# Kernel optimization log

Measured on AMD Instinct MI355X. Metric: run time of the kernel, lower is better.

The kernel has to match this reference:

```python
import jax, jax.numpy as jnp
import numpy as np

N = 10000
E = 320000
IN_DIM = 256
HID = 128
HEADS = 3
NEG_SLOPE = 0.2
EPS = 1e-8


def setup_inputs() -> dict:
    key = jax.random.key(0)
    ks = jax.random.split(key, 12)
    rn = lambda k, s, sc=0.1: jax.random.normal(k, s, dtype=jnp.float32) * sc
    return {
        'x1': jax.random.normal(ks[0], (N, IN_DIM), dtype=jnp.float32),
        'edge_index1': jax.random.randint(ks[1], (2, E), 0, N, dtype=jnp.int64),
        'x2': jax.random.normal(ks[2], (N, IN_DIM), dtype=jnp.float32),
        'edge_index2': jax.random.randint(ks[3], (2, E), 0, N, dtype=jnp.int64),
        'W1': rn(ks[4], (IN_DIM, HEADS * HID)),
        'att_src1': rn(ks[5], (HEADS, HID)),
        'att_dst1': rn(ks[6], (HEADS, HID)),
        'b1': rn(ks[7], (HEADS * HID,)),
        'W2': rn(ks[8], (HEADS * HID, HID)),
        'att_src2': rn(ks[9], (1, HID)),
        'att_dst2': rn(ks[10], (1, HID)),
        'b2': rn(ks[11], (HID,)),
    }


def gat_conv(x, edge_index, W, a_src, a_dst, bias, heads, out_ch, concat):
    """PyG-style GATConv with add_self_loops=True."""
    n = x.shape[0]
    loops = jnp.arange(n, dtype=edge_index.dtype)
    ei = jnp.concatenate([edge_index, jnp.stack([loops, loops])], axis=1)
    src, dst = ei[0], ei[1]
    h = (x @ W).reshape(n, heads, out_ch)                    # [N,H,C]
    s = jnp.einsum('nhc,hc->nh', h, a_src)                    # alpha_src per node
    d = jnp.einsum('nhc,hc->nh', h, a_dst)                    # alpha_dst per node
    e = jax.nn.leaky_relu(s[src] + d[dst], NEG_SLOPE)         # [Etot,H]
    m = jax.ops.segment_max(e, dst, num_segments=n)           # segment softmax (stable)
    ex = jnp.exp(e - m[dst])
    denom = jax.ops.segment_sum(ex, dst, num_segments=n)
    alpha = ex / denom[dst]                                   # [Etot,H]
    out = jax.ops.segment_sum(h[src] * alpha[:, :, None], dst, num_segments=n)
    out = out.reshape(n, heads * out_ch) if concat else out.mean(axis=1)
    return out + bias, (ei, alpha)


def _branch(x, ei, W1, as1, ad1, b1, W2, as2, ad2, b2):
    e1, (ei_sl, alpha1) = gat_conv(x, ei, W1, as1, ad1, b1, HEADS, HID, True)
    e1 = jax.nn.relu(e1)
    e2, _ = gat_conv(e1, ei, W2, as2, ad2, b2, 1, HID, False)
    # _graph_pooling
    attn_val = alpha1.mean(axis=1)                            # [Etot]
    node_attn = jax.ops.segment_sum(attn_val, ei_sl[1], num_segments=x.shape[0])
    weighted = e2 * node_attn[:, None]
    pooled = jnp.concatenate([weighted.mean(axis=0), e2.mean(axis=0)])  # [2*HID]
    return pooled, alpha1


def reference(x1, edge_index1, x2, edge_index2, W1, att_src1, att_dst1, b1,
              W2, att_src2, att_dst2, b2):
    g1, alpha1 = _branch(x1, edge_index1, W1, att_src1, att_dst1, b1,
                         W2, att_src2, att_dst2, b2)
    g2, alpha2 = _branch(x2, edge_index2, W1, att_src1, att_dst1, b1,
                         W2, att_src2, att_dst2, b2)
    n1 = jnp.maximum(jnp.linalg.norm(g1), EPS)
    n2 = jnp.maximum(jnp.linalg.norm(g2), EPS)
    sim = jnp.dot(g1, g2) / (n1 * n2)
    return sim, alpha1, alpha2
```

## Files before the change

### kernel.cpp

```cpp
#include <hip/hip_runtime.h>
#include <hip/hip_bf16.h>
#include <cstdint>
#include <cstddef>

#define INDIM 256
#define NEG 0.2f

typedef __attribute__((ext_vector_type(8))) short short8v;
typedef __attribute__((ext_vector_type(4))) float f32x4;
typedef __attribute__((ext_vector_type(2))) float f32x2;

__device__ __forceinline__ unsigned short f2bf(float x) {
  __hip_bfloat16 b = __float2bfloat16(x);
  return __builtin_bit_cast(unsigned short, b);
}

__device__ __forceinline__ unsigned char f2fp8(float v) {
  int packed = __builtin_amdgcn_cvt_pk_fp8_f32(v, v, 0, false);
  return (unsigned char)(packed & 0xff);
}

__device__ __forceinline__ float lrelu(float v) { return v > 0.f ? v : NEG * v; }

__global__ void wprep_kernel(const float* __restrict__ W1, __hip_bfloat16* __restrict__ W1t,
                             const float* __restrict__ W2, __hip_bfloat16* __restrict__ W2t) {
  int idx = blockIdx.x * blockDim.x + threadIdx.x;
  const int T1 = 256 * 384;
  if (idx < T1) {
    int k = idx / 384, c = idx - k * 384;
    W1t[(size_t)c * 256 + k] = __float2bfloat16(W1[idx]);
  } else {
    int i = idx - T1;
    if (i < 384 * 128) {
      int k = i / 128, c = i - k * 128;
      W2t[(size_t)c * 384 + k] = __float2bfloat16(W2[i]);
    }
  }
}

template<int K, bool ABF16, int SST>
__device__ __forceinline__ void gemm_body(int bx, int by,
                                          const void* __restrict__ A0,
                                          const void* __restrict__ A1, int Nsplit,
                                          const __hip_bfloat16* __restrict__ Wt,
                                          const float* __restrict__ att_s,
                                          const float* __restrict__ att_d,
                                          unsigned char* __restrict__ Yc,
                                          float* __restrict__ So,
                                          float* __restrict__ Do,
                                          int M, int NC,
                                          short (*As)[40], short (*Bs)[40],
                                          float (*sred)[64]) {
  const int tid = threadIdx.x;
  const int row0 = bx * 64;
  const int col0 = by * 128;
  const int l = tid & 63, w = tid >> 6;
  const int wr = w >> 1, wc = w & 1;
  const int lr = l & 15, lk = (l >> 4) * 8;

  f32x4 acc[2][4];
#pragma unroll
  for (int m = 0; m < 2; ++m)
#pragma unroll
    for (int n = 0; n < 4; ++n) acc[m][n] = {0.f, 0.f, 0.f, 0.f};

  for (int k0 = 0; k0 < K; k0 += 32) {
    __syncthreads();
    {
      int r = tid >> 2, kq = (tid & 3) * 8;
      int gr = row0 + r;
      short8v av = {0, 0, 0, 0, 0, 0, 0, 0};
      if (gr < M) {
        const void* Ab = (gr < Nsplit) ? A0 : A1;
        int lrow = (gr < Nsplit) ? gr : gr - Nsplit;
        if (ABF16) {
          av = *(const short8v*)((const short*)Ab + (size_t)lrow * K + k0 + kq);
        } else {
          const float* ap = (const float*)Ab + (size_t)lrow * K + k0 + kq;
          float4 u = *(const float4*)ap;
          float4 v = *(const float4*)(ap + 4);
          av = short8v{(short)f2bf(u.x), (short)f2bf(u.y), (short)f2bf(u.z), (short)f2bf(u.w),
                       (short)f2bf(v.x), (short)f2bf(v.y), (short)f2bf(v.z), (short)f2bf(v.w)};
        }
      }
      *(short8v*)&As[r][kq] = av;
    }
    {
      int c = tid >> 1, kq = (tid & 1) * 8;
      const short* wp = (const short*)Wt + (size_t)(col0 + c) * K + k0 + kq;
      *(short8v*)&Bs[c][kq]      = *(const short8v*)wp;
      *(short8v*)&Bs[c][kq + 16] = *(const short8v*)(wp + 16);
    }
    __syncthreads();
    short8v a[2], b[4];
#pragma unroll
    for (int m = 0; m < 2; ++m) a[m] = *(short8v*)&As[wr * 32 + m * 16 + lr][lk];
#pragma unroll
    for (int n = 0; n < 4; ++n) b[n] = *(short8v*)&Bs[wc * 64 + n * 16 + lr][lk];
#pragma unroll
    for (int m = 0; m < 2; ++m)
#pragma unroll
      for (int n = 0; n < 4; ++n)
        acc[m][n] = __builtin_amdgcn_mfma_f32_16x16x32_bf16(a[m], b[n], acc[m][n], 0, 0, 0);
  }
#pragma unroll
  for (int m = 0; m < 2; ++m) {
    int rbase = row0 + wr * 32 + m * 16 + (l >> 4) * 4;
#pragma unroll
    for (int n = 0; n < 4; ++n) {
      int col = col0 + wc * 64 + n * 16 + lr;
#pragma unroll
      for (int q = 0; q < 4; ++q) {
        int row = rbase + q;
        if (row < M) Yc[(size_t)row * NC + col] = f2fp8(acc[m][n][q]);
      }
    }
  }
  float asv[4], adv[4];
#pragma unroll
  for (int n = 0; n < 4; ++n) {
    int col = col0 + wc * 64 + n * 16 + lr;
    asv[n] = att_s[col];
    adv[n] = att_d[col];
  }
  float ps[2][4], pd[2][4];
#pragma unroll
  for (int m = 0; m < 2; ++m)
#pragma unroll
    for (int q = 0; q < 4; ++q) {
      float s = 0.f, d = 0.f;
#pragma unroll
      for (int n = 0; n < 4; ++n) {
        s = fmaf(acc[m][n][q], asv[n], s);
        d = fmaf(acc[m][n][q], adv[n], d);
      }
      ps[m][q] = s; pd[m][q] = d;
    }
#pragma unroll
  for (int o = 1; o < 16; o <<= 1) {
#pragma unroll
    for (int m = 0; m < 2; ++m)
#pragma unroll
      for (int q = 0; q < 4; ++q) {
        ps[m][q] += __shfl_xor(ps[m][q], o);
        pd[m][q] += __shfl_xor(pd[m][q], o);
      }
  }
  __syncthreads();
  if (wc == 1 && lr == 0) {
#pragma unroll
    for (int m = 0; m < 2; ++m)
#pragma unroll
      for (int q = 0; q < 4; ++q) {
        int rl = wr * 32 + m * 16 + (l >> 4) * 4 + q;
        sred[0][rl] = ps[m][q];
        sred[1][rl] = pd[m][q];
      }
  }
  __syncthreads();
  if (wc == 0 && lr == 0) {
#pragma unroll
    for (int m = 0; m < 2; ++m)
#pragma unroll
      for (int q = 0; q < 4; ++q) {
        int rl = wr * 32 + m * 16 + (l >> 4) * 4 + q;
        int row = row0 + rl;
        if (row < M) {
          So[(size_t)row * SST + by] = ps[m][q] + sred[0][rl];
          Do[(size_t)row * SST + by] = pd[m][q] + sred[1][rl];
        }
      }
  }
}

__global__ __launch_bounds__(256) void gemm1_deg_kernel(const float* __restrict__ x1,
                                                        const float* __restrict__ x2, int Nsplit,
                                                        const __hip_bfloat16* __restrict__ Wt,
                                                        const float* __restrict__ att_s,
                                                        const float* __restrict__ att_d,
                                                        unsigned char* __restrict__ Yc,
                                                        float* __restrict__ So,
                                                        float* __restrict__ Do,
                                                        int M, int gmx,
                                                        const int* __restrict__ ed1,
                                                        const int* __restrict__ ed2,
                                                        int E, int Etot, int N,
                                                        int* __restrict__ deg) {
  __shared__ short As[64][40];
  __shared__ short Bs[128][40];
  __shared__ float sred[2][64];
  int bid = blockIdx.x;
  if (bid < gmx * 3) {
    gemm_body<256, false, 4>(bid % gmx, bid / gmx, x1, x2, Nsplit, Wt, att_s, att_d,
                             Yc, So, Do, M, 384, As, Bs, sred);
  } else {
    int idx = (bid - gmx * 3) * 256 + threadIdx.x;
    if (idx < 2 * Etot) {
      int br = idx >= Etot;
      int el = idx - br * Etot;
      const int* ed = br ? ed2 : ed1;
      int dn = ((el < E) ? ed[el] : (el - E)) + br * N;
      atomicAdd(&deg[dn], 1);
    }
  }
}

__global__ __launch_bounds__(256) void gemm2_alpha_kernel(const __hip_bfloat16* __restrict__ e1b,
                                                          const __hip_bfloat16* __restrict__ Wt,
                                                          const float* __restrict__ att_s,
                                                          const float* __restrict__ att_d,
                                                          unsigned char* __restrict__ Yc,
                                                          float* __restrict__ So,
                                                          float* __restrict__ Do,
                                                          int M, int gmx,
                                                          const float* __restrict__ S4,
                                                          const float* __restrict__ D4,
                                                          const float* __restrict__ invden,
                                                          const int* __restrict__ es1,
                                                          const int* __restrict__ ed1,
                                                          const int* __restrict__ es2,
                                                          const int* __restrict__ ed2,
                                                          int E, int Etot, int N,
                                                          float* __restrict__ out) {
  __shared__ short As[64][40];
  __shared__ short Bs[128][40];
  __shared__ float sred[2][64];
  int bid = blockIdx.x;
  if (bid < gmx) {
    gemm_body<384, true, 1>(bid, 0, e1b, e1b, M, Wt, att_s, att_d,
                            Yc, So, Do, M, 128, As, Bs, sred);
  } else {
    int idx = (bid - gmx) * 256 + threadIdx.x;
    if (idx < 2 * Etot) {
      int br = idx >= Etot;
      int el = idx - br * Etot;
      const int* es = br ? es2 : es1;
      const int* ed = br ? ed2 : ed1;
      int sn, dn;
      if (el < E) { sn = es[el]; dn = ed[el]; } else { sn = dn = el - E; }
      sn += br * N; dn += br * N;
      float* ao = out + 1 + (size_t)br * Etot * 3 + (size_t)el * 3;
#pragma unroll
      for (int h = 0; h < 3; ++h) {
        float v = lrelu(S4[sn * 4 + h] + D4[dn * 4 + h]);
        ao[h] = __expf(v) * invden[dn * 3 + h];
      }
    }
  }
}

__global__ __launch_bounds__(1024) void scan_kernel(const int* __restrict__ deg,
                                                    int* __restrict__ rowptr,
                                                    int* __restrict__ cursor, int n) {
  __shared__ int wsum[16];
  int t = threadIdx.x, lane = t & 63, wid = t >> 6;
  int start = t * 20;
  int v[20];
  int s = 0;
#pragma unroll
  for (int k = 0; k < 20; ++k) {
    int i = start + k;
    int d = (i < n) ? deg[i] : 0;
    s += d;
    v[k] = s;
  }
  int x = s;
#pragma unroll
  for (int o = 1; o < 64; o <<= 1) {
    int tm = __shfl_up(x, o);
    if (lane >= o) x += tm;
  }
  if (lane == 63) wsum[wid] = x;
  __syncthreads();
  if (wid == 0) {
    int wv = (lane < 16) ? wsum[lane] : 0;
#pragma unroll
    for (int o = 1; o < 16; o <<= 1) {
      int tm = __shfl_up(wv, o);
      if (lane >= o) wv += tm;
    }
    if (lane < 16) wsum[lane] = wv;
  }
  __syncthreads();
  int excl = (x - s) + (wid ? wsum[wid - 1] : 0);
  if (t == 0) rowptr[0] = 0;
#pragma unroll
  for (int k = 0; k < 20; ++k) {
    int i = start + k;
    if (i < n) {
      rowptr[i + 1] = excl + v[k];
      cursor[i] = excl + (k ? v[k - 1] : 0);
    }
  }
}

__global__ void fill_kernel(const int* __restrict__ es1, const int* __restrict__ ed1,
                            const int* __restrict__ es2, const int* __restrict__ ed2,
                            int E, int Etot, int N, int* __restrict__ cursor,
                            int* __restrict__ csr_src) {
  int idx = blockIdx.x * blockDim.x + threadIdx.x;
  if (idx >= 2 * Etot) return;
  int br = idx >= Etot;
  int el = idx - br * Etot;
  const int* es = br ? es2 : es1;
  const int* ed = br ? ed2 : ed1;
  int sn, dn;
  if (el < E) { sn = es[el]; dn = ed[el]; } else { sn = dn = el - E; }
  sn += br * N; dn += br * N;
  int pos = atomicAdd(&cursor[dn], 1);
  csr_src[pos] = sn;
}

__global__ __launch_bounds__(256) void agg1_kernel(const unsigned char* __restrict__ h1c,
                                                   const float* __restrict__ S4,
                                                   const float* __restrict__ D4,
                                                   const int* __restrict__ rowptr,
                                                   const int* __restrict__ csr_src,
                                                   const float* __restrict__ b1,
                                                   __hip_bfloat16* __restrict__ e1b,
                                                   float* __restrict__ invden, int N2) {
  __shared__ float4 st[4][64];
  int wv = threadIdx.x >> 6;
  int n = blockIdx.x * 4 + wv;
  if (n >= N2) return;
  int l = threadIdx.x & 63;
  int head = l >> 5;
  const float4* S4v = reinterpret_cast<const float4*>(S4);
  int p0 = rowptr[n], p1 = rowptr[n + 1];
  float d0 = D4[n * 4], d1 = D4[n * 4 + 1], d2 = D4[n * 4 + 2];

  float dp0 = 0.f, dp1 = 0.f, dp2 = 0.f;
  float acc[6] = {0.f, 0.f, 0.f, 0.f, 0.f, 0.f};
  for (int base = p0; base < p1; base += 64) {
    int cnt = min(64, p1 - base);
    if (l < cnt) {
      int sn = csr_src[base + l];
      float4 sv = S4v[sn];
      float e0 = __expf(lrelu(sv.x + d0));
      float e1 = __expf(lrelu(sv.y + d1));
      float e2 = __expf(lrelu(sv.z + d2));
      st[wv][l] = make_float4(__int_as_float(sn), e0, e1, e2);
      dp0 += e0; dp1 += e1; dp2 += e2;
    }
    int i = 0;
    for (; i + 4 <= cnt; i += 4) {
      float4 w[4];
      unsigned int hv[4];
      unsigned short gv[4];
#pragma unroll
      for (int u = 0; u < 4; ++u) {
        w[u] = st[wv][i + u];
        int sn = __float_as_int(w[u].x);
        const unsigned char* row = h1c + (size_t)sn * 384;
        hv[u] = *reinterpret_cast<const unsigned int*>(row + 4 * l);
        gv[u] = *reinterpret_cast<const unsigned short*>(row + 256 + 2 * l);
      }
#pragma unroll
      for (int u = 0; u < 4; ++u) {
        float alo = head ? w[u].z : w[u].y;
        float ahi = w[u].w;
        f32x2 f0 = __builtin_amdgcn_cvt_pk_f32_fp8((int)hv[u], false);
        f32x2 f1 = __builtin_amdgcn_cvt_pk_f32_fp8((int)hv[u], true);
        f32x2 g0 = __builtin_amdgcn_cvt_pk_f32_fp8((int)(unsigned int)gv[u], false);
        acc[0] = fmaf(alo, f0.x, acc[0]);
        acc[1] = fmaf(alo, f0.y, acc[1]);
        acc[2] = fmaf(alo, f1.x, acc[2]);
        acc[3] = fmaf(alo, f1.y, acc[3]);
        acc[4] = fmaf(ahi, g0.x, acc[4]);
        acc[5] = fmaf(ahi, g0.y, acc[5]);
      }
    }
    for (; i < cnt; ++i) {
      float4 w = st[wv][i];
      int sn = __float_as_int(w.x);
      const unsigned char* row = h1c + (size_t)sn * 384;
      unsigned int hv = *reinterpret_cast<const unsigned int*>(row + 4 * l);
      unsigned short gv = *reinterpret_cast<const unsigned short*>(row + 256 + 2 * l);
      float alo = head ? w.z : w.y;
      float ahi = w.w;
      f32x2 f0 = __builtin_amdgcn_cvt_pk_f32_fp8((int)hv, false);
      f32x2 f1 = __builtin_amdgcn_cvt_pk_f32_fp8((int)hv, true);
      f32x2 g0 = __builtin_amdgcn_cvt_pk_f32_fp8((int)(unsigned int)gv, false);
      acc[0] = fmaf(alo, f0.x, acc[0]);
      acc[1] = fmaf(alo, f0.y, acc[1]);
      acc[2] = fmaf(alo, f1.x, acc[2]);
      acc[3] = fmaf(alo, f1.y, acc[3]);
      acc[4] = fmaf(ahi, g0.x, acc[4]);
      acc[5] = fmaf(ahi, g0.y, acc[5]);
    }
  }
#pragma unroll
  for (int o = 32; o; o >>= 1) {
    dp0 += __shfl_down(dp0, o); dp1 += __shfl_down(dp1, o); dp2 += __shfl_down(dp2, o);
  }
  float inv0 = 1.f / __shfl(dp0, 0);
  float inv1 = 1.f / __shfl(dp1, 0);
  float inv2 = 1.f / __shfl(dp2, 0);

  float ilo = head ? inv1 : inv0;
  int c0 = 4 * l;
  float4 bb = *reinterpret_cast<const float4*>(b1 + c0);
  float v0 = acc[0] * ilo + bb.x;
  float v1 = acc[1] * ilo + bb.y;
  float v2 = acc[2] * ilo + bb.z;
  float v3 = acc[3] * ilo + bb.w;
  v0 = v0 > 0.f ? v0 : 0.f; v1 = v1 > 0.f ? v1 : 0.f;
  v2 = v2 > 0.f ? v2 : 0.f; v3 = v3 > 0.f ? v3 : 0.f;
  int ch = 256 + 2 * l;
  float2 bh = *reinterpret_cast<const float2*>(b1 + ch);
  float v4 = acc[4] * inv2 + bh.x;
  float v5 = acc[5] * inv2 + bh.y;
  v4 = v4 > 0.f ? v4 : 0.f; v5 = v5 > 0.f ? v5 : 0.f;
  unsigned short* eb = reinterpret_cast<unsigned short*>(e1b) + (size_t)n * 384;
  uint2 lo;
  lo.x = (unsigned int)f2bf(v0) | ((unsigned int)f2bf(v1) << 16);
  lo.y = (unsigned int)f2bf(v2) | ((unsigned int)f2bf(v3) << 16);
  *reinterpret_cast<uint2*>(eb + c0) = lo;
  *reinterpret_cast<unsigned int*>(eb + ch) =
      (unsigned int)f2bf(v4) | ((unsigned int)f2bf(v5) << 16);
  if (l == 0) invden[n * 3] = inv0;
  else if (l == 1) invden[n * 3 + 1] = inv1;
  else if (l == 2) invden[n * 3 + 2] = inv2;
}

__global__ __launch_bounds__(256) void agg2_kernel(const unsigned char* __restrict__ h2c,
                                                   const float* __restrict__ S2,
                                                   const float* __restrict__ D2,
                                                   const int* __restrict__ rowptr,
                                                   const int* __restrict__ csr_src,
                                                   const float* __restrict__ b2,
                                                   float* __restrict__ e2out, int N2) {
  __shared__ int lsrc[4][256];
  __shared__ float la[4][256];
  const unsigned int* H4 = reinterpret_cast<const unsigned int*>(h2c);
  int wv = threadIdx.x >> 6;
  int n = blockIdx.x * 4 + wv;
  if (n >= N2) return;
  int lane = threadIdx.x & 63;
  int half = lane >> 5, t = lane & 31;
  int p0 = rowptr[n], p1 = rowptr[n + 1];
  float dnv = D2[n];

  float dpart = 0.f;
  float acc[4] = {0.f, 0.f, 0.f, 0.f};
  for (int base = p0; base < p1; base += 256) {
    int cnt = min(256, p1 - base);
    for (int i = lane; i < cnt; i += 64) {
      int sn = csr_src[base + i];
      lsrc[wv][i] = sn;
      float ex = __expf(lrelu(S2[sn] + dnv));
      la[wv][i] = ex;
      dpart += ex;
    }
    int i = half;
    for (; i + 14 < cnt; i += 16) {
      unsigned int hv[8];
      float av[8];
#pragma unroll
      for (int u = 0; u < 8; ++u) {
        int e = i + 2 * u;
        int sn = lsrc[wv][e];
        av[u] = la[wv][e];
        hv[u] = H4[(size_t)sn * 32 + t];
      }
#pragma unroll
      for (int u = 0; u < 8; ++u) {
        f32x2 f0 = __builtin_amdgcn_cvt_pk_f32_fp8((int)hv[u], false);
        f32x2 f1 = __builtin_amdgcn_cvt_pk_f32_fp8((int)hv[u], true);
        acc[0] = fmaf(av[u], f0.x, acc[0]);
        acc[1] = fmaf(av[u], f0.y, acc[1]);
        acc[2] = fmaf(av[u], f1.x, acc[2]);
        acc[3] = fmaf(av[u], f1.y, acc[3]);
      }
    }
    for (; i < cnt; i += 2) {
      int sn = lsrc[wv][i];
      float a = la[wv][i];
      unsigned int hv = H4[(size_t)sn * 32 + t];
      f32x2 f0 = __builtin_amdgcn_cvt_pk_f32_fp8((int)hv, false);
      f32x2 f1 = __builtin_amdgcn_cvt_pk_f32_fp8((int)hv, true);
      acc[0] = fmaf(a, f0.x, acc[0]);
      acc[1] = fmaf(a, f0.y, acc[1]);
      acc[2] = fmaf(a, f1.x, acc[2]);
      acc[3] = fmaf(a, f1.y, acc[3]);
    }
  }
#pragma unroll
  for (int k = 0; k < 4; ++k) acc[k] += __shfl_xor(acc[k], 32);
#pragma unroll
  for (int o = 32; o; o >>= 1) dpart += __shfl_down(dpart, o);
  float invden = 1.f / __shfl(dpart, 0);
  if (half == 0) {
    float4 bb = *reinterpret_cast<const float4*>(b2 + 4 * t);
    float4 ov;
    ov.x = acc[0] * invden + bb.x;
    ov.y = acc[1] * invden + bb.y;
    ov.z = acc[2] * invden + bb.z;
    ov.w = acc[3] * invden + bb.w;
    *reinterpret_cast<float4*>(e2out + (size_t)n * 128 + 4 * t) = ov;
  }
}

__global__ __launch_bounds__(128) void pool_sim_kernel(const float* __restrict__ e2,
                                                       float* __restrict__ g,
                                                       int* __restrict__ cnt,
                                                       int N, float invN,
                                                       float* __restrict__ out) {
  int c = threadIdx.x;
  int br = blockIdx.y;
  int r0 = br * N + blockIdx.x * 128;
  int r1 = min(r0 + 128, br * N + N);
  float acc = 0.f;
  for (int n = r0; n < r1; ++n) acc += e2[(size_t)n * 128 + c];
  atomicAdd(&g[br * 128 + c], acc * invN);
  __threadfence();
  __shared__ bool last;
  __shared__ float sd[128], s1[128], s2[128];
  if (c == 0) {
    int total = gridDim.x * gridDim.y;
    last = (atomicAdd(cnt, 1) == total - 1);
  }
  __syncthreads();
  if (!last) return;
  float a = atomicAdd(&g[c], 0.f);
  float b = atomicAdd(&g[128 + c], 0.f);
  sd[c] = a * b; s1[c] = a * a; s2[c] = b * b;
  __syncthreads();
  for (int ofs = 64; ofs; ofs >>= 1) {
    if (c < ofs) { sd[c] += sd[c + ofs]; s1[c] += s1[c + ofs]; s2[c] += s2[c + ofs]; }
    __syncthreads();
  }
  if (c == 0) {
    float n1 = fmaxf(sqrtf(s1[0]), 1e-8f);
    float n2 = fmaxf(sqrtf(s2[0]), 1e-8f);
    out[0] = sd[0] / (n1 * n2);
  }
}

extern "C" void kernel_launch(void* const* d_in, const int* in_sizes, int n_in,
                              void* d_out, int out_size, void* d_ws, size_t ws_size,
                              hipStream_t stream) {
  const int N = in_sizes[0] / INDIM;
  const int E = in_sizes[1] / 2;
  const int Etot = E + N;
  const int N2 = 2 * N;

  const float* x1  = (const float*)d_in[0];
  const int*   ei1 = (const int*)d_in[1];
  const float* x2  = (const float*)d_in[2];
  const int*   ei2 = (const int*)d_in[3];
  const float* W1  = (const float*)d_in[4];
  const float* as1 = (const float*)d_in[5];
  const float* ad1 = (const float*)d_in[6];
  const float* b1  = (const float*)d_in[7];
  const float* W2  = (const float*)d_in[8];
  const float* as2 = (const float*)d_in[9];
  const float* ad2 = (const float*)d_in[10];
  const float* b2  = (const float*)d_in[11];
  float* out = (float*)d_out;
  const int* es1 = ei1, *ed1 = ei1 + E;
  const int* es2 = ei2, *ed2 = ei2 + E;

  char* p = (char*)d_ws;
  auto alloc = [&](size_t bytes) -> char* {
    char* q = p;
    p += (bytes + 255) & ~(size_t)255;
    return q;
  };
  float* g   = (float*)alloc(256 * 4);
  int*   cnt = (int*)alloc(256);
  int*   deg = (int*)alloc((size_t)N2 * 4);
  size_t zero_bytes = (size_t)((char*)deg - (char*)g) + (((size_t)N2 * 4 + 255) & ~(size_t)255);

  unsigned char* h1c = (unsigned char*)alloc((size_t)N2 * 384);
  __hip_bfloat16* e1b = (__hip_bfloat16*)alloc((size_t)N2 * 384 * 2);
  unsigned char* h2c = (unsigned char*)alloc((size_t)N2 * 128);
  float* e2          = (float*)alloc((size_t)N2 * 128 * 4);
  __hip_bfloat16* W1t = (__hip_bfloat16*)alloc((size_t)256 * 384 * 2);
  __hip_bfloat16* W2t = (__hip_bfloat16*)alloc((size_t)384 * 128 * 2);
  float* s1v  = (float*)alloc((size_t)N2 * 4 * 4);
  float* d1v  = (float*)alloc((size_t)N2 * 4 * 4);
  float* s2v  = (float*)alloc((size_t)N2 * 4);
  float* d2v  = (float*)alloc((size_t)N2 * 4);
  float* idn  = (float*)alloc((size_t)N2 * 3 * 4);
  int* rowptr  = (int*)alloc((size_t)(N2 + 1) * 4);
  int* cursor  = (int*)alloc((size_t)N2 * 4);
  int* csr_src = (int*)alloc((size_t)2 * Etot * 4);

  const int EB = 256;
  const int egrid2 = (2 * Etot + EB - 1) / EB;
  const int gmx = (N2 + 63) / 64;

  hipMemsetAsync(g, 0, zero_bytes, stream);
  wprep_kernel<<<(256 * 384 + 384 * 128 + 255) / 256, 256, 0, stream>>>(W1, W1t, W2, W2t);

  gemm1_deg_kernel<<<gmx * 3 + egrid2, 256, 0, stream>>>(x1, x2, N, W1t, as1, ad1,
                                                         h1c, s1v, d1v, N2, gmx,
                                                         ed1, ed2, E, Etot, N, deg);
  scan_kernel<<<1, 1024, 0, stream>>>(deg, rowptr, cursor, N2);
  fill_kernel<<<egrid2, EB, 0, stream>>>(es1, ed1, es2, ed2, E, Etot, N, cursor, csr_src);

  agg1_kernel<<<(N2 + 3) / 4, 256, 0, stream>>>(h1c, s1v, d1v, rowptr, csr_src, b1,
                                                e1b, idn, N2);

  gemm2_alpha_kernel<<<gmx + egrid2, 256, 0, stream>>>(e1b, W2t, as2, ad2,
                                                       h2c, s2v, d2v, N2, gmx,
                                                       s1v, d1v, idn,
                                                       es1, ed1, es2, ed2, E, Etot, N, out);
  agg2_kernel<<<(N2 + 3) / 4, 256, 0, stream>>>(h2c, s2v, d2v, rowptr, csr_src, b2, e2, N2);

  pool_sim_kernel<<<dim3((N + 127) / 128, 2), 128, 0, stream>>>(e2, g, cnt, N,
                                                                1.f / (float)N, out);
}
```

Measured before the change: 220.8 us.

## Widen GEMM1 tile to all 384 columns and fold edge work into GEMM blocks

GEMM1 now has each block compute a full 64x384 output tile, so the x rows are loaded and converted to bf16 once instead of once per 128-column group. Head-wise attention dot products are split across the two column-half warps with a shared-memory reduction. Both fused kernels drop the separate edge-work blocks. Every GEMM block now first runs a grid-stride loop over the degree-count or alpha edge work before its GEMM. This cuts the grid to gmx blocks but uses more registers and LDS in GEMM1, which may lower occupancy, and serialises the edge work ahead of the matrix math in each block.

```diff
diff --git a/kernel.cpp b/kernel.cpp
--- a/kernel.cpp
+++ b/kernel.cpp
@@ -38,141 +38,6 @@
   }
 }
 
-template<int K, bool ABF16, int SST>
-__device__ __forceinline__ void gemm_body(int bx, int by,
-                                          const void* __restrict__ A0,
-                                          const void* __restrict__ A1, int Nsplit,
-                                          const __hip_bfloat16* __restrict__ Wt,
-                                          const float* __restrict__ att_s,
-                                          const float* __restrict__ att_d,
-                                          unsigned char* __restrict__ Yc,
-                                          float* __restrict__ So,
-                                          float* __restrict__ Do,
-                                          int M, int NC,
-                                          short (*As)[40], short (*Bs)[40],
-                                          float (*sred)[64]) {
-  const int tid = threadIdx.x;
-  const int row0 = bx * 64;
-  const int col0 = by * 128;
-  const int l = tid & 63, w = tid >> 6;
-  const int wr = w >> 1, wc = w & 1;
-  const int lr = l & 15, lk = (l >> 4) * 8;
-
-  f32x4 acc[2][4];
-#pragma unroll
-  for (int m = 0; m < 2; ++m)
-#pragma unroll
-    for (int n = 0; n < 4; ++n) acc[m][n] = {0.f, 0.f, 0.f, 0.f};
-
-  for (int k0 = 0; k0 < K; k0 += 32) {
-    __syncthreads();
-    {
-      int r = tid >> 2, kq = (tid & 3) * 8;
-      int gr = row0 + r;
-      short8v av = {0, 0, 0, 0, 0, 0, 0, 0};
-      if (gr < M) {
-        const void* Ab = (gr < Nsplit) ? A0 : A1;
-        int lrow = (gr < Nsplit) ? gr : gr - Nsplit;
-        if (ABF16) {
-          av = *(const short8v*)((const short*)Ab + (size_t)lrow * K + k0 + kq);
-        } else {
-          const float* ap = (const float*)Ab + (size_t)lrow * K + k0 + kq;
-          float4 u = *(const float4*)ap;
-          float4 v = *(const float4*)(ap + 4);
-          av = short8v{(short)f2bf(u.x), (short)f2bf(u.y), (short)f2bf(u.z), (short)f2bf(u.w),
-                       (short)f2bf(v.x), (short)f2bf(v.y), (short)f2bf(v.z), (short)f2bf(v.w)};
-        }
-      }
-      *(short8v*)&As[r][kq] = av;
-    }
-    {
-      int c = tid >> 1, kq = (tid & 1) * 8;
-      const short* wp = (const short*)Wt + (size_t)(col0 + c) * K + k0 + kq;
-      *(short8v*)&Bs[c][kq]      = *(const short8v*)wp;
-      *(short8v*)&Bs[c][kq + 16] = *(const short8v*)(wp + 16);
-    }
-    __syncthreads();
-    short8v a[2], b[4];
-#pragma unroll
-    for (int m = 0; m < 2; ++m) a[m] = *(short8v*)&As[wr * 32 + m * 16 + lr][lk];
-#pragma unroll
-    for (int n = 0; n < 4; ++n) b[n] = *(short8v*)&Bs[wc * 64 + n * 16 + lr][lk];
-#pragma unroll
-    for (int m = 0; m < 2; ++m)
-#pragma unroll
-      for (int n = 0; n < 4; ++n)
-        acc[m][n] = __builtin_amdgcn_mfma_f32_16x16x32_bf16(a[m], b[n], acc[m][n], 0, 0, 0);
-  }
-#pragma unroll
-  for (int m = 0; m < 2; ++m) {
-    int rbase = row0 + wr * 32 + m * 16 + (l >> 4) * 4;
-#pragma unroll
-    for (int n = 0; n < 4; ++n) {
-      int col = col0 + wc * 64 + n * 16 + lr;
-#pragma unroll
-      for (int q = 0; q < 4; ++q) {
-        int row = rbase + q;
-        if (row < M) Yc[(size_t)row * NC + col] = f2fp8(acc[m][n][q]);
-      }
-    }
-  }
-  float asv[4], adv[4];
-#pragma unroll
-  for (int n = 0; n < 4; ++n) {
-    int col = col0 + wc * 64 + n * 16 + lr;
-    asv[n] = att_s[col];
-    adv[n] = att_d[col];
-  }
-  float ps[2][4], pd[2][4];
-#pragma unroll
-  for (int m = 0; m < 2; ++m)
-#pragma unroll
-    for (int q = 0; q < 4; ++q) {
-      float s = 0.f, d = 0.f;
-#pragma unroll
-      for (int n = 0; n < 4; ++n) {
-        s = fmaf(acc[m][n][q], asv[n], s);
-        d = fmaf(acc[m][n][q], adv[n], d);
-      }
-      ps[m][q] = s; pd[m][q] = d;
-    }
-#pragma unroll
-  for (int o = 1; o < 16; o <<= 1) {
-#pragma unroll
-    for (int m = 0; m < 2; ++m)
-#pragma unroll
-      for (int q = 0; q < 4; ++q) {
-        ps[m][q] += __shfl_xor(ps[m][q], o);
-        pd[m][q] += __shfl_xor(pd[m][q], o);
-      }
-  }
-  __syncthreads();
-  if (wc == 1 && lr == 0) {
-#pragma unroll
-    for (int m = 0; m < 2; ++m)
-#pragma unroll
-      for (int q = 0; q < 4; ++q) {
-        int rl = wr * 32 + m * 16 + (l >> 4) * 4 + q;
-        sred[0][rl] = ps[m][q];
-        sred[1][rl] = pd[m][q];
-      }
-  }
-  __syncthreads();
-  if (wc == 0 && lr == 0) {
-#pragma unroll
-    for (int m = 0; m < 2; ++m)
-#pragma unroll
-      for (int q = 0; q < 4; ++q) {
-        int rl = wr * 32 + m * 16 + (l >> 4) * 4 + q;
-        int row = row0 + rl;
-        if (row < M) {
-          So[(size_t)row * SST + by] = ps[m][q] + sred[0][rl];
-          Do[(size_t)row * SST + by] = pd[m][q] + sred[1][rl];
-        }
-      }
-  }
-}
-
 __global__ __launch_bounds__(256) void gemm1_deg_kernel(const float* __restrict__ x1,
                                                         const float* __restrict__ x2, int Nsplit,
                                                         const __hip_bfloat16* __restrict__ Wt,
@@ -181,27 +46,149 @@
                                                         unsigned char* __restrict__ Yc,
                                                         float* __restrict__ So,
                                                         float* __restrict__ Do,
-                                                        int M, int gmx,
+                                                        int M,
                                                         const int* __restrict__ ed1,
                                                         const int* __restrict__ ed2,
                                                         int E, int Etot, int N,
                                                         int* __restrict__ deg) {
   __shared__ short As[64][40];
-  __shared__ short Bs[128][40];
-  __shared__ float sred[2][64];
-  int bid = blockIdx.x;
-  if (bid < gmx * 3) {
-    gemm_body<256, false, 4>(bid % gmx, bid / gmx, x1, x2, Nsplit, Wt, att_s, att_d,
-                             Yc, So, Do, M, 384, As, Bs, sred);
-  } else {
-    int idx = (bid - gmx * 3) * 256 + threadIdx.x;
-    if (idx < 2 * Etot) {
-      int br = idx >= Etot;
-      int el = idx - br * Etot;
-      const int* ed = br ? ed2 : ed1;
-      int dn = ((el < E) ? ed[el] : (el - E)) + br * N;
-      atomicAdd(&deg[dn], 1);
-    }
+  __shared__ short Bs[384][40];
+  __shared__ float sred[4][64];
+  const int tid = threadIdx.x;
+
+  for (int idx = blockIdx.x * 256 + tid; idx < 2 * Etot; idx += gridDim.x * 256) {
+    int br = idx >= Etot;
+    int el = idx - br * Etot;
+    const int* ed = br ? ed2 : ed1;
+    int dn = ((el < E) ? ed[el] : (el - E)) + br * N;
+    atomicAdd(&deg[dn], 1);
+  }
+
+  const int row0 = blockIdx.x * 64;
+  const int l = tid & 63, w = tid >> 6;
+  const int wr = w >> 1, wc = w & 1;
+  const int lr = l & 15, lk = (l >> 4) * 8;
+
+  f32x4 acc[2][12];
+#pragma unroll
+  for (int m = 0; m < 2; ++m)
+#pragma unroll
+    for (int n = 0; n < 12; ++n) acc[m][n] = {0.f, 0.f, 0.f, 0.f};
+
+  for (int k0 = 0; k0 < 256; k0 += 32) {
+    __syncthreads();
+    {
+      int r = tid >> 2, kq = (tid & 3) * 8;
+      int gr = row0 + r;
+      short8v av = {0, 0, 0, 0, 0, 0, 0, 0};
+      if (gr < M) {
+        const float* base = (gr < Nsplit) ? x1 : x2;
+        int lrow = (gr < Nsplit) ? gr : gr - Nsplit;
+        const float* ap = base + (size_t)lrow * 256 + k0 + kq;
+        float4 u = *(const float4*)ap;
+        float4 v = *(const float4*)(ap + 4);
+        av = short8v{(short)f2bf(u.x), (short)f2bf(u.y), (short)f2bf(u.z), (short)f2bf(u.w),
+                     (short)f2bf(v.x), (short)f2bf(v.y), (short)f2bf(v.z), (short)f2bf(v.w)};
+      }
+      *(short8v*)&As[r][kq] = av;
+    }
+    {
+#pragma unroll
+      for (int j = 0; j < 6; ++j) {
+        int id = tid + j * 256;
+        int c = id >> 2, kq = (id & 3) * 8;
+        *(short8v*)&Bs[c][kq] = *(const short8v*)(Wt + (size_t)c * 256 + k0 + kq);
+      }
+    }
+    __syncthreads();
+    short8v a0 = *(short8v*)&As[wr * 32 + lr][lk];
+    short8v a1 = *(short8v*)&As[wr * 32 + 16 + lr][lk];
+#pragma unroll
+    for (int n = 0; n < 12; ++n) {
+      short8v b = *(short8v*)&Bs[wc * 192 + n * 16 + lr][lk];
+      acc[0][n] = __builtin_amdgcn_mfma_f32_16x16x32_bf16(a0, b, acc[0][n], 0, 0, 0);
+      acc[1][n] = __builtin_amdgcn_mfma_f32_16x16x32_bf16(a1, b, acc[1][n], 0, 0, 0);
+    }
+  }
+#pragma unroll
+  for (int m = 0; m < 2; ++m) {
+    int rbase = row0 + wr * 32 + m * 16 + (l >> 4) * 4;
+#pragma unroll
+    for (int n = 0; n < 12; ++n) {
+      int col = wc * 192 + n * 16 + lr;
+#pragma unroll
+      for (int q = 0; q < 4; ++q) {
+        int row = rbase + q;
+        if (row < M) Yc[(size_t)row * 384 + col] = f2fp8(acc[m][n][q]);
+      }
+    }
+  }
+  float psA[2][4] = {}, pdA[2][4] = {}, psB[2][4] = {}, pdB[2][4] = {};
+  const int nsplit = wc ? 4 : 8;
+#pragma unroll
+  for (int n = 0; n < 12; ++n) {
+    int col = wc * 192 + n * 16 + lr;
+    float as_ = att_s[col];
+    float ad_ = att_d[col];
+    if (n < nsplit) {
+#pragma unroll
+      for (int m = 0; m < 2; ++m)
+#pragma unroll
+        for (int q = 0; q < 4; ++q) {
+          psA[m][q] = fmaf(acc[m][n][q], as_, psA[m][q]);
+          pdA[m][q] = fmaf(acc[m][n][q], ad_, pdA[m][q]);
+        }
+    } else {
+#pragma unroll
+      for (int m = 0; m < 2; ++m)
+#pragma unroll
+        for (int q = 0; q < 4; ++q) {
+          psB[m][q] = fmaf(acc[m][n][q], as_, psB[m][q]);
+          pdB[m][q] = fmaf(acc[m][n][q], ad_, pdB[m][q]);
+        }
+    }
+  }
+#pragma unroll
+  for (int o = 1; o < 16; o <<= 1) {
+#pragma unroll
+    for (int m = 0; m < 2; ++m)
+#pragma unroll
+      for (int q = 0; q < 4; ++q) {
+        psA[m][q] += __shfl_xor(psA[m][q], o);
+        pdA[m][q] += __shfl_xor(pdA[m][q], o);
+        psB[m][q] += __shfl_xor(psB[m][q], o);
+        pdB[m][q] += __shfl_xor(pdB[m][q], o);
+      }
+  }
+  if (wc == 1 && lr == 0) {
+#pragma unroll
+    for (int m = 0; m < 2; ++m)
+#pragma unroll
+      for (int q = 0; q < 4; ++q) {
+        int rl = wr * 32 + m * 16 + (l >> 4) * 4 + q;
+        sred[0][rl] = psA[m][q];
+        sred[1][rl] = pdA[m][q];
+        sred[2][rl] = psB[m][q];
+        sred[3][rl] = pdB[m][q];
+      }
+  }
+  __syncthreads();
+  if (wc == 0 && lr == 0) {
+#pragma unroll
+    for (int m = 0; m < 2; ++m)
+#pragma unroll
+      for (int q = 0; q < 4; ++q) {
+        int rl = wr * 32 + m * 16 + (l >> 4) * 4 + q;
+        int row = row0 + rl;
+        if (row < M) {
+          So[(size_t)row * 4 + 0] = psA[m][q];
+          Do[(size_t)row * 4 + 0] = pdA[m][q];
+          So[(size_t)row * 4 + 1] = psB[m][q] + sred[0][rl];
+          Do[(size_t)row * 4 + 1] = pdB[m][q] + sred[1][rl];
+          So[(size_t)row * 4 + 2] = sred[2][rl];
+          Do[(size_t)row * 4 + 2] = sred[3][rl];
+        }
+      }
   }
 }
 
@@ -212,7 +199,7 @@
                                                           unsigned char* __restrict__ Yc,
                                                           float* __restrict__ So,
                                                           float* __restrict__ Do,
-                                                          int M, int gmx,
+                                                          int M,
                                                           const float* __restrict__ S4,
                                                           const float* __restrict__ D4,
                                                           const float* __restrict__ invden,
@@ -225,27 +212,128 @@
   __shared__ short As[64][40];
   __shared__ short Bs[128][40];
   __shared__ float sred[2][64];
-  int bid = blockIdx.x;
-  if (bid < gmx) {
-    gemm_body<384, true, 1>(bid, 0, e1b, e1b, M, Wt, att_s, att_d,
-                            Yc, So, Do, M, 128, As, Bs, sred);
-  } else {
-    int idx = (bid - gmx) * 256 + threadIdx.x;
-    if (idx < 2 * Etot) {
-      int br = idx >= Etot;
-      int el = idx - br * Etot;
-      const int* es = br ? es2 : es1;
-      const int* ed = br ? ed2 : ed1;
-      int sn, dn;
-      if (el < E) { sn = es[el]; dn = ed[el]; } else { sn = dn = el - E; }
-      sn += br * N; dn += br * N;
-      float* ao = out + 1 + (size_t)br * Etot * 3 + (size_t)el * 3;
-#pragma unroll
-      for (int h = 0; h < 3; ++h) {
-        float v = lrelu(S4[sn * 4 + h] + D4[dn * 4 + h]);
-        ao[h] = __expf(v) * invden[dn * 3 + h];
-      }
-    }
+  const int tid = threadIdx.x;
+
+  for (int idx = blockIdx.x * 256 + tid; idx < 2 * Etot; idx += gridDim.x * 256) {
+    int br = idx >= Etot;
+    int el = idx - br * Etot;
+    const int* es = br ? es2 : es1;
+    const int* ed = br ? ed2 : ed1;
+    int sn, dn;
+    if (el < E) { sn = es[el]; dn = ed[el]; } else { sn = dn = el - E; }
+    sn += br * N; dn += br * N;
+    float* ao = out + 1 + (size_t)br * Etot * 3 + (size_t)el * 3;
+#pragma unroll
+    for (int h = 0; h < 3; ++h) {
+      float v = lrelu(S4[sn * 4 + h] + D4[dn * 4 + h]);
+      ao[h] = __expf(v) * invden[dn * 3 + h];
+    }
+  }
+
+  const int row0 = blockIdx.x * 64;
+  const int l = tid & 63, w = tid >> 6;
+  const int wr = w >> 1, wc = w & 1;
+  const int lr = l & 15, lk = (l >> 4) * 8;
+
+  f32x4 acc[2][4];
+#pragma unroll
+  for (int m = 0; m < 2; ++m)
+#pragma unroll
+    for (int n = 0; n < 4; ++n) acc[m][n] = {0.f, 0.f, 0.f, 0.f};
+
+  for (int k0 = 0; k0 < 384; k0 += 32) {
+    __syncthreads();
+    {
+      int r = tid >> 2, kq = (tid & 3) * 8;
+      int gr = row0 + r;
+      short8v av = {0, 0, 0, 0, 0, 0, 0, 0};
+      if (gr < M) av = *(const short8v*)((const short*)e1b + (size_t)gr * 384 + k0 + kq);
+      *(short8v*)&As[r][kq] = av;
+    }
+    {
+      int c = tid >> 1, kq = (tid & 1) * 8;
+      const short* wp = (const short*)Wt + (size_t)c * 384 + k0 + kq;
+      *(short8v*)&Bs[c][kq]      = *(const short8v*)wp;
+      *(short8v*)&Bs[c][kq + 16] = *(const short8v*)(wp + 16);
+    }
+    __syncthreads();
+    short8v a[2], b[4];
+#pragma unroll
+    for (int m = 0; m < 2; ++m) a[m] = *(short8v*)&As[wr * 32 + m * 16 + lr][lk];
+#pragma unroll
+    for (int n = 0; n < 4; ++n) b[n] = *(short8v*)&Bs[wc * 64 + n * 16 + lr][lk];
+#pragma unroll
+    for (int m = 0; m < 2; ++m)
+#pragma unroll
+      for (int n = 0; n < 4; ++n)
+        acc[m][n] = __builtin_amdgcn_mfma_f32_16x16x32_bf16(a[m], b[n], acc[m][n], 0, 0, 0);
+  }
+#pragma unroll
+  for (int m = 0; m < 2; ++m) {
+    int rbase = row0 + wr * 32 + m * 16 + (l >> 4) * 4;
+#pragma unroll
+    for (int n = 0; n < 4; ++n) {
+      int col = wc * 64 + n * 16 + lr;
+#pragma unroll
+      for (int q = 0; q < 4; ++q) {
+        int row = rbase + q;
+        if (row < M) Yc[(size_t)row * 128 + col] = f2fp8(acc[m][n][q]);
+      }
+    }
+  }
+  float asv[4], adv[4];
+#pragma unroll
+  for (int n = 0; n < 4; ++n) {
+    int col = wc * 64 + n * 16 + lr;
+    asv[n] = att_s[col];
+    adv[n] = att_d[col];
+  }
+  float ps[2][4], pd[2][4];
+#pragma unroll
+  for (int m = 0; m < 2; ++m)
+#pragma unroll
+    for (int q = 0; q < 4; ++q) {
+      float s = 0.f, d = 0.f;
+#pragma unroll
+      for (int n = 0; n < 4; ++n) {
+        s = fmaf(acc[m][n][q], asv[n], s);
+        d = fmaf(acc[m][n][q], adv[n], d);
+      }
+      ps[m][q] = s; pd[m][q] = d;
+    }
+#pragma unroll
+  for (int o = 1; o < 16; o <<= 1) {
+#pragma unroll
+    for (int m = 0; m < 2; ++m)
+#pragma unroll
+      for (int q = 0; q < 4; ++q) {
+        ps[m][q] += __shfl_xor(ps[m][q], o);
+        pd[m][q] += __shfl_xor(pd[m][q], o);
+      }
+  }
+  if (wc == 1 && lr == 0) {
+#pragma unroll
+    for (int m = 0; m < 2; ++m)
+#pragma unroll
+      for (int q = 0; q < 4; ++q) {
+        int rl = wr * 32 + m * 16 + (l >> 4) * 4 + q;
+        sred[0][rl] = ps[m][q];
+        sred[1][rl] = pd[m][q];
+      }
+  }
+  __syncthreads();
+  if (wc == 0 && lr == 0) {
+#pragma unroll
+    for (int m = 0; m < 2; ++m)
+#pragma unroll
+      for (int q = 0; q < 4; ++q) {
+        int rl = wr * 32 + m * 16 + (l >> 4) * 4 + q;
+        int row = row0 + rl;
+        if (row < M) {
+          So[row] = ps[m][q] + sred[0][rl];
+          Do[row] = pd[m][q] + sred[1][rl];
+        }
+      }
   }
 }
 
@@ -594,19 +682,19 @@
   hipMemsetAsync(g, 0, zero_bytes, stream);
   wprep_kernel<<<(256 * 384 + 384 * 128 + 255) / 256, 256, 0, stream>>>(W1, W1t, W2, W2t);
 
-  gemm1_deg_kernel<<<gmx * 3 + egrid2, 256, 0, stream>>>(x1, x2, N, W1t, as1, ad1,
-                                                         h1c, s1v, d1v, N2, gmx,
-                                                         ed1, ed2, E, Etot, N, deg);
+  gemm1_deg_kernel<<<gmx, 256, 0, stream>>>(x1, x2, N, W1t, as1, ad1,
+                                            h1c, s1v, d1v, N2,
+                                            ed1, ed2, E, Etot, N, deg);
   scan_kernel<<<1, 1024, 0, stream>>>(deg, rowptr, cursor, N2);
   fill_kernel<<<egrid2, EB, 0, stream>>>(es1, ed1, es2, ed2, E, Etot, N, cursor, csr_src);
 
   agg1_kernel<<<(N2 + 3) / 4, 256, 0, stream>>>(h1c, s1v, d1v, rowptr, csr_src, b1,
                                                 e1b, idn, N2);
 
-  gemm2_alpha_kernel<<<gmx + egrid2, 256, 0, stream>>>(e1b, W2t, as2, ad2,
-                                                       h2c, s2v, d2v, N2, gmx,
-                                                       s1v, d1v, idn,
-                                                       es1, ed1, es2, ed2, E, Etot, N, out);
+  gemm2_alpha_kernel<<<gmx, 256, 0, stream>>>(e1b, W2t, as2, ad2,
+                                              h2c, s2v, d2v, N2,
+                                              s1v, d1v, idn,
+                                              es1, ed1, es2, ed2, E, Etot, N, out);
   agg2_kernel<<<(N2 + 3) / 4, 256, 0, stream>>>(h2c, s2v, d2v, rowptr, csr_src, b2, e2, N2);
 
   pool_sim_kernel<<<dim3((N + 127) / 128, 2), 128, 0, stream>>>(e2, g, cnt, N,
```

Result: slower. 248.7 us (+12.7%).
